# Kernel optimization log

Measured on AMD Instinct MI355X. Metric: run time of the kernel, lower is better.

Reference implementation:

```python
import jax, jax.numpy as jnp
import numpy as np

INPUT_DIM, HIDDEN_DIM, OUTPUT_DIM = 60, 256, 402


def setup_inputs() -> dict:
    key = jax.random.key(0)
    ks = jax.random.split(key, 7)
    B, T, J, D = 64, 512, 20, 3
    s_ih = 1.0 / np.sqrt(HIDDEN_DIM)
    return {
        "x": jax.random.normal(ks[0], (B, T, J, D), dtype=jnp.float32),
        "W_ih": jax.random.uniform(ks[1], (4 * HIDDEN_DIM, INPUT_DIM), minval=-s_ih, maxval=s_ih, dtype=jnp.float32),
        "W_hh": jax.random.uniform(ks[2], (4 * HIDDEN_DIM, HIDDEN_DIM), minval=-s_ih, maxval=s_ih, dtype=jnp.float32),
        "b_ih": jax.random.uniform(ks[3], (4 * HIDDEN_DIM,), minval=-s_ih, maxval=s_ih, dtype=jnp.float32),
        "b_hh": jax.random.uniform(ks[4], (4 * HIDDEN_DIM,), minval=-s_ih, maxval=s_ih, dtype=jnp.float32),
        "W_fc": jax.random.uniform(ks[5], (OUTPUT_DIM, HIDDEN_DIM), minval=-s_ih, maxval=s_ih, dtype=jnp.float32),
        "b_fc": jax.random.uniform(ks[6], (OUTPUT_DIM,), minval=-s_ih, maxval=s_ih, dtype=jnp.float32),
    }


def _lstm(x, W_ih, W_hh, b_ih, b_hh):
    # x: [B, T, INPUT_DIM] -> hidden states [B, T, H]
    B = x.shape[0]
    H = W_hh.shape[1]
    # Precompute input contribution to all gates for the whole sequence (one big GEMM)
    xg = jnp.einsum('bti,gi->btg', x, W_ih) + b_ih + b_hh  # [B, T, 4H]

    def step(carry, xt):
        h, c = carry
        gates = xt + h @ W_hh.T  # [B, 4H]; pytorch gate order: i, f, g, o
        i, f, g, o = jnp.split(gates, 4, axis=-1)
        i = jax.nn.sigmoid(i)
        f = jax.nn.sigmoid(f)
        g = jnp.tanh(g)
        o = jax.nn.sigmoid(o)
        c = f * c + i * g
        h = o * jnp.tanh(c)
        return (h, c), h

    h0 = jnp.zeros((B, H), dtype=x.dtype)
    (_, _), hs = jax.lax.scan(step, (h0, h0), jnp.swapaxes(xg, 0, 1))  # hs: [T, B, H]
    return jnp.swapaxes(hs, 0, 1)


def reference(x, W_ih, W_hh, b_ih, b_hh, W_fc, b_fc):
    B, T, J, D = x.shape
    xf = x.reshape(B, T, J * D)
    hs = _lstm(xf, W_ih, W_hh, b_ih, b_hh)  # [B, T, H]
    out = jnp.einsum('bth,oh->bto', hs, W_fc) + b_fc  # [B, T, OUTPUT_DIM]
    return out
```

## Files before the change

kernel.cpp:

```cpp
#include <hip/hip_runtime.h>
#include <hip/hip_fp16.h>

typedef _Float16 half2v __attribute__((ext_vector_type(2)));

#define B_ 64
#define T_ 512
#define H_ 256
#define G4_ 1024
#define IN_ 60
#define O_ 402

__device__ __forceinline__ float fdot2(unsigned int a, unsigned int b, float c) {
  return __builtin_amdgcn_fdot2(__builtin_bit_cast(half2v, a),
                                __builtin_bit_cast(half2v, b), c, false);
}

__device__ __forceinline__ unsigned int pack_h2(float a, float b) {
  unsigned short ua = __half_as_ushort(__float2half(a));
  unsigned short ub = __half_as_ushort(__float2half(b));
  return (unsigned int)ua | ((unsigned int)ub << 16);
}

__device__ __forceinline__ float sigmoid_f(float x) {
  return __fdividef(1.0f, 1.0f + __expf(-x));
}
__device__ __forceinline__ float tanh_f(float x) {
  float ax = fminf(fabsf(x) * 2.0f, 40.0f);
  float e = __expf(ax);
  float r = __fdividef(e - 1.0f, e + 1.0f);
  return copysignf(r, x);
}

__global__ __launch_bounds__(256) void k0_pack(
    const float* __restrict__ wih, const float* __restrict__ whh,
    const float* __restrict__ bih, const float* __restrict__ bhh,
    const float* __restrict__ wfc,
    float* __restrict__ wpih, float* __restrict__ biasp,
    unsigned int* __restrict__ wreg_ws, unsigned int* __restrict__ wlds_ws,
    unsigned int* __restrict__ wfcp) {
  int idx = blockIdx.x * 256 + threadIdx.x;
  if (idx < 61440) {
    int k = idx / 1024, rp = idx % 1024;
    int orig = (rp & 3) * 256 + (rp >> 2);
    wpih[idx] = wih[orig * IN_ + k];
  } else if (idx < 62464) {
    int rp = idx - 61440;
    int orig = (rp & 3) * 256 + (rp >> 2);
    biasp[rp] = bih[orig] + bhh[orig];
  } else if (idx < 193536) {
    int i2 = idx - 62464;
    int l = i2 >> 8;
    int i = i2 & 255;
    int cc = i >> 4, q = (i >> 2) & 3, p = i & 3;
    int u = l >> 1, hf = l & 1;
    int P = hf * 64 + cc * 4 + p;
    int row = q * 256 + u;
    unsigned int pk = pack_h2(whh[row * 256 + 2 * P], whh[row * 256 + 2 * P + 1]);
    if (cc < 12) wreg_ws[((cc * 4 + q) * 512 + l) * 4 + p] = pk;
    else         wlds_ws[(((cc - 12) * 4 + q) * 512 + l) * 4 + p] = pk;
  } else if (idx < 244992) {
    int i3 = idx - 193536;
    int o = i3 >> 7, P = i3 & 127;
    wfcp[o * 128 + P] = pack_h2(wfc[o * 256 + 2 * P], wfc[o * 256 + 2 * P + 1]);
  }
}

template <bool F32>
__global__ __launch_bounds__(256, 2) void k1_xgemm(
    const float* __restrict__ x, const float* __restrict__ wpih,
    const float* __restrict__ biasp, void* __restrict__ xg_v) {
  __shared__ float xt[IN_ * 64];
  const int l = threadIdx.x, blk = blockIdx.x;
  for (int i = l; i < IN_ * 64; i += 256) {
    int k = i >> 6, bt = i & 63;
    xt[i] = x[(size_t)(blk * 64 + bt) * IN_ + k];
  }
  __syncthreads();
  float4 bias4 = *(const float4*)&biasp[4 * l];
  float* xg_f = (float*)xg_v;
  unsigned int* xg_h = (unsigned int*)xg_v;
  for (int half = 0; half < 2; ++half) {
    float4 a[32];
#pragma unroll
    for (int j = 0; j < 32; ++j) a[j] = bias4;
    for (int k = 0; k < IN_; ++k) {
      float4 w4 = *(const float4*)&wpih[k * G4_ + 4 * l];
#pragma unroll
      for (int j4 = 0; j4 < 8; ++j4) {
        float4 xv = *(const float4*)&xt[k * 64 + half * 32 + j4 * 4];
        float xs[4] = {xv.x, xv.y, xv.z, xv.w};
#pragma unroll
        for (int jj = 0; jj < 4; ++jj) {
          float xc = xs[jj];
          float4& A = a[j4 * 4 + jj];
          A.x = fmaf(w4.x, xc, A.x); A.y = fmaf(w4.y, xc, A.y);
          A.z = fmaf(w4.z, xc, A.z); A.w = fmaf(w4.w, xc, A.w);
        }
      }
    }
#pragma unroll
    for (int j = 0; j < 32; ++j) {
      size_t bt = (size_t)blk * 64 + half * 32 + j;
      if constexpr (F32) {
        *(float4*)&xg_f[bt * G4_ + 4 * l] = a[j];
      } else {
        uint2 pk;
        pk.x = pack_h2(a[j].x, a[j].y);
        pk.y = pack_h2(a[j].z, a[j].w);
        *(uint2*)&xg_h[bt * (G4_ / 2) + 2 * l] = pk;
      }
    }
  }
}

template <bool F32>
__global__ __launch_bounds__(512, 2) void k2_lstm(
    const void* __restrict__ xg_v, const uint4* __restrict__ wreg_ws,
    const uint4* __restrict__ wlds_ws, unsigned short* __restrict__ hs) {
  __shared__ uint4 wlds[4 * 4 * 512];
  __shared__ __align__(16) unsigned short hbuf[2][256];
  const int l = threadIdx.x;
  const int b = blockIdx.x;
  const int u = l >> 1, hf = l & 1;
  for (int i = l; i < 4 * 4 * 512; i += 512) wlds[i] = wlds_ws[i];
  if (l < 128) ((unsigned int*)hbuf)[l] = 0u;

  uint4 wr[48];
#pragma unroll
  for (int i = 0; i < 48; ++i) wr[i] = wreg_ws[i * 512 + l];

  const float4* xg4 = (const float4*)xg_v;
  const uint2*  xg2 = (const uint2*)xg_v;
  float4 xf; uint2 xh;
  if constexpr (F32) xf = xg4[(size_t)b * T_ * 256 + u];
  else               xh = xg2[(size_t)b * T_ * 256 + u];
  float c = 0.0f;
  __syncthreads();
  for (int t = 0; t < T_; ++t) {
    float a0, a1, a2, a3;
    if constexpr (F32) {
      a0 = hf ? 0.0f : xf.x; a1 = hf ? 0.0f : xf.y;
      a2 = hf ? 0.0f : xf.z; a3 = hf ? 0.0f : xf.w;
    } else {
      half2v p0 = __builtin_bit_cast(half2v, xh.x);
      half2v p1 = __builtin_bit_cast(half2v, xh.y);
      a0 = hf ? 0.0f : (float)p0[0]; a1 = hf ? 0.0f : (float)p0[1];
      a2 = hf ? 0.0f : (float)p1[0]; a3 = hf ? 0.0f : (float)p1[1];
    }
    int tn = (t < T_ - 1) ? (t + 1) : t;
    if constexpr (F32) xf = xg4[(size_t)(b * T_ + tn) * 256 + u];
    else               xh = xg2[(size_t)(b * T_ + tn) * 256 + u];

    const uint4* hB = (const uint4*)(&hbuf[t & 1][hf * 128]);
#pragma unroll
    for (int cc = 0; cc < 16; ++cc) {
      uint4 hq = hB[cc];
      uint4 w0, w1, w2, w3;
      if (cc < 12) {
        w0 = wr[cc * 4 + 0]; w1 = wr[cc * 4 + 1];
        w2 = wr[cc * 4 + 2]; w3 = wr[cc * 4 + 3];
      } else {
        int c2 = cc - 12;
        w0 = wlds[(c2 * 4 + 0) * 512 + l];
        w1 = wlds[(c2 * 4 + 1) * 512 + l];
        w2 = wlds[(c2 * 4 + 2) * 512 + l];
        w3 = wlds[(c2 * 4 + 3) * 512 + l];
      }
      a0 = fdot2(w0.x, hq.x, a0); a0 = fdot2(w0.y, hq.y, a0);
      a0 = fdot2(w0.z, hq.z, a0); a0 = fdot2(w0.w, hq.w, a0);
      a1 = fdot2(w1.x, hq.x, a1); a1 = fdot2(w1.y, hq.y, a1);
      a1 = fdot2(w1.z, hq.z, a1); a1 = fdot2(w1.w, hq.w, a1);
      a2 = fdot2(w2.x, hq.x, a2); a2 = fdot2(w2.y, hq.y, a2);
      a2 = fdot2(w2.z, hq.z, a2); a2 = fdot2(w2.w, hq.w, a2);
      a3 = fdot2(w3.x, hq.x, a3); a3 = fdot2(w3.y, hq.y, a3);
      a3 = fdot2(w3.z, hq.z, a3); a3 = fdot2(w3.w, hq.w, a3);
    }
    a0 += __shfl_xor(a0, 1); a1 += __shfl_xor(a1, 1);
    a2 += __shfl_xor(a2, 1); a3 += __shfl_xor(a3, 1);
    float ig = sigmoid_f(a0), fg = sigmoid_f(a1);
    float gg = tanh_f(a2),    og = sigmoid_f(a3);
    c = fg * c + ig * gg;
    float h = og * tanh_f(c);
    unsigned short hbits = __half_as_ushort(__float2half(h));
    if (hf == 0) {
      hbuf[(t & 1) ^ 1][u] = hbits;
      hs[(size_t)(b * T_ + t) * H_ + u] = hbits;
    }
    __syncthreads();
  }
}

__global__ __launch_bounds__(256, 2) void k3_out(
    const unsigned short* __restrict__ hs, const unsigned int* __restrict__ wfcp,
    const float* __restrict__ bfc, float* __restrict__ out) {
  __shared__ unsigned int ht[64 * 128];
  const int l = threadIdx.x, blk = blockIdx.x;
  const unsigned int* hsrc = (const unsigned int*)hs + (size_t)blk * 64 * 128;
  for (int i = l; i < 64 * 128; i += 256) ht[i] = hsrc[i];
  __syncthreads();
  const int c1 = l;
  const int c2 = 256 + l;
  const bool has2 = (c2 < O_);
  const int c2r = has2 ? c2 : 0;
  float b1 = bfc[c1], b2 = bfc[c2r];
  for (int btc = 0; btc < 4; ++btc) {
    float a1[16], a2[16];
#pragma unroll
    for (int j = 0; j < 16; ++j) { a1[j] = b1; a2[j] = b2; }
    for (int Pc = 0; Pc < 8; ++Pc) {
      uint4 wq1[4], wq2[4];
#pragma unroll
      for (int p4 = 0; p4 < 4; ++p4) {
        wq1[p4] = *(const uint4*)&wfcp[c1 * 128 + Pc * 16 + 4 * p4];
        wq2[p4] = *(const uint4*)&wfcp[c2r * 128 + Pc * 16 + 4 * p4];
      }
#pragma unroll
      for (int j = 0; j < 16; ++j) {
        const unsigned int* hr = &ht[(btc * 16 + j) * 128 + Pc * 16];
#pragma unroll
        for (int p4 = 0; p4 < 4; ++p4) {
          uint4 hv = *(const uint4*)&hr[4 * p4];
          a1[j] = fdot2(wq1[p4].x, hv.x, a1[j]);
          a1[j] = fdot2(wq1[p4].y, hv.y, a1[j]);
          a1[j] = fdot2(wq1[p4].z, hv.z, a1[j]);
          a1[j] = fdot2(wq1[p4].w, hv.w, a1[j]);
          a2[j] = fdot2(wq2[p4].x, hv.x, a2[j]);
          a2[j] = fdot2(wq2[p4].y, hv.y, a2[j]);
          a2[j] = fdot2(wq2[p4].z, hv.z, a2[j]);
          a2[j] = fdot2(wq2[p4].w, hv.w, a2[j]);
        }
      }
    }
#pragma unroll
    for (int j = 0; j < 16; ++j) {
      size_t bt = (size_t)blk * 64 + btc * 16 + j;
      out[bt * O_ + c1] = a1[j];
      if (has2) out[bt * O_ + c2] = a2[j];
    }
  }
}

extern "C" void kernel_launch(void* const* d_in, const int* in_sizes, int n_in,
                              void* d_out, int out_size, void* d_ws, size_t ws_size,
                              hipStream_t stream) {
  const float* x   = (const float*)d_in[0];
  const float* wih = (const float*)d_in[1];
  const float* whh = (const float*)d_in[2];
  const float* bih = (const float*)d_in[3];
  const float* bhh = (const float*)d_in[4];
  const float* wfc = (const float*)d_in[5];
  const float* bfc = (const float*)d_in[6];
  float* out = (float*)d_out;
  char* ws = (char*)d_ws;

  const size_t HS_BYTES = (size_t)B_ * T_ * H_ * 2;
  const size_t XG_F32   = (size_t)B_ * T_ * G4_ * 4;
  const size_t WREG_B   = 12 * 4 * 512 * 16;
  const size_t WLDS_B   = 4 * 4 * 512 * 16;
  const size_t WPIH_B   = (size_t)IN_ * G4_ * 4;
  const size_t BIAS_B   = (size_t)G4_ * 4;
  const size_t WFCP_B   = (size_t)O_ * 128 * 4;
  const size_t TAIL = HS_BYTES + WREG_B + WLDS_B + WPIH_B + BIAS_B + WFCP_B;

  bool f32xg = (ws_size >= XG_F32 + TAIL);
  size_t xg_bytes = f32xg ? XG_F32 : ((size_t)B_ * T_ * G4_ * 2);

  char* xg    = ws;
  char* hsb   = ws + xg_bytes;
  char* wregp = hsb + HS_BYTES;
  char* wldsp = wregp + WREG_B;
  char* wpihp = wldsp + WLDS_B;
  char* biasp = wpihp + WPIH_B;
  char* wfcpp = biasp + BIAS_B;

  hipLaunchKernelGGL(k0_pack, dim3(957), dim3(256), 0, stream,
                     wih, whh, bih, bhh, wfc,
                     (float*)wpihp, (float*)biasp,
                     (unsigned int*)wregp, (unsigned int*)wldsp,
                     (unsigned int*)wfcpp);
  if (f32xg) {
    hipLaunchKernelGGL((k1_xgemm<true>), dim3(512), dim3(256), 0, stream,
                       x, (const float*)wpihp, (const float*)biasp, (void*)xg);
    hipLaunchKernelGGL((k2_lstm<true>), dim3(64), dim3(512), 0, stream,
                       (const void*)xg, (const uint4*)wregp, (const uint4*)wldsp,
                       (unsigned short*)hsb);
  } else {
    hipLaunchKernelGGL((k1_xgemm<false>), dim3(512), dim3(256), 0, stream,
                       x, (const float*)wpihp, (const float*)biasp, (void*)xg);
    hipLaunchKernelGGL((k2_lstm<false>), dim3(64), dim3(512), 0, stream,
                       (const void*)xg, (const uint4*)wregp, (const uint4*)wldsp,
                       (unsigned short*)hsb);
  }
  hipLaunchKernelGGL(k3_out, dim3(512), dim3(256), 0, stream,
                     (const unsigned short*)hsb, (const unsigned int*)wfcpp,
                     bfc, out);
}
```

Measured before the change: 981.5 us.

## Hold recurrent weights in AGPRs, rebalance LDS split, pack hidden-state writes

```diff
diff --git a/kernel.cpp b/kernel.cpp
--- a/kernel.cpp
+++ b/kernel.cpp
@@ -9,6 +9,9 @@
 #define G4_ 1024
 #define IN_ 60
 #define O_ 402
+
+#define NREGQ 45
+#define NLDSQ 19
 
 __device__ __forceinline__ float fdot2(unsigned int a, unsigned int b, float c) {
   return __builtin_amdgcn_fdot2(__builtin_bit_cast(half2v, a),
@@ -51,13 +54,14 @@
     int i2 = idx - 62464;
     int l = i2 >> 8;
     int i = i2 & 255;
-    int cc = i >> 4, q = (i >> 2) & 3, p = i & 3;
+    int jq = i >> 2, p = i & 3;
+    int cc = jq >> 2, q = jq & 3;
     int u = l >> 1, hf = l & 1;
     int P = hf * 64 + cc * 4 + p;
     int row = q * 256 + u;
     unsigned int pk = pack_h2(whh[row * 256 + 2 * P], whh[row * 256 + 2 * P + 1]);
-    if (cc < 12) wreg_ws[((cc * 4 + q) * 512 + l) * 4 + p] = pk;
-    else         wlds_ws[(((cc - 12) * 4 + q) * 512 + l) * 4 + p] = pk;
+    if (jq < NREGQ) wreg_ws[(jq * 512 + l) * 4 + p] = pk;
+    else            wlds_ws[((jq - NREGQ) * 512 + l) * 4 + p] = pk;
   } else if (idx < 244992) {
     int i3 = idx - 193536;
     int o = i3 >> 7, P = i3 & 127;
@@ -117,63 +121,71 @@
 __global__ __launch_bounds__(512, 2) void k2_lstm(
     const void* __restrict__ xg_v, const uint4* __restrict__ wreg_ws,
     const uint4* __restrict__ wlds_ws, unsigned short* __restrict__ hs) {
-  __shared__ uint4 wlds[4 * 4 * 512];
-  __shared__ __align__(16) unsigned short hbuf[2][256];
+  __shared__ uint4 wlds[NLDSQ * 512];
+  __shared__ unsigned int hq4[2][2][68];
   const int l = threadIdx.x;
   const int b = blockIdx.x;
   const int u = l >> 1, hf = l & 1;
-  for (int i = l; i < 4 * 4 * 512; i += 512) wlds[i] = wlds_ws[i];
-  if (l < 128) ((unsigned int*)hbuf)[l] = 0u;
-
-  uint4 wr[48];
-#pragma unroll
-  for (int i = 0; i < 48; ++i) wr[i] = wreg_ws[i * 512 + l];
-
-  const float4* xg4 = (const float4*)xg_v;
-  const uint2*  xg2 = (const uint2*)xg_v;
-  float4 xf; uint2 xh;
-  if constexpr (F32) xf = xg4[(size_t)b * T_ * 256 + u];
-  else               xh = xg2[(size_t)b * T_ * 256 + u];
+  for (int i = l; i < NLDSQ * 512; i += 512) wlds[i] = wlds_ws[i];
+  if (l < 64)        hq4[0][0][l] = 0u;
+  else if (l < 128)  hq4[0][1][l - 64] = 0u;
+
+  unsigned int wa[NREGQ * 4];
+#pragma unroll
+  for (int j = 0; j < NREGQ; ++j) {
+    uint4 v = wreg_ws[j * 512 + l];
+    asm("v_accvgpr_write_b32 %0, %1" : "=a"(wa[4 * j + 0]) : "v"(v.x));
+    asm("v_accvgpr_write_b32 %0, %1" : "=a"(wa[4 * j + 1]) : "v"(v.y));
+    asm("v_accvgpr_write_b32 %0, %1" : "=a"(wa[4 * j + 2]) : "v"(v.z));
+    asm("v_accvgpr_write_b32 %0, %1" : "=a"(wa[4 * j + 3]) : "v"(v.w));
+  }
+
+  const unsigned int* xgu = (const unsigned int*)xg_v;
+  const float2* xgf2 = (const float2*)xg_v;
+  float2 xf2; unsigned int xh;
+  if constexpr (F32) xf2 = xgf2[(size_t)b * T_ * 512 + l];
+  else               xh  = xgu[(size_t)b * T_ * 512 + l];
   float c = 0.0f;
   __syncthreads();
   for (int t = 0; t < T_; ++t) {
-    float a0, a1, a2, a3;
-    if constexpr (F32) {
-      a0 = hf ? 0.0f : xf.x; a1 = hf ? 0.0f : xf.y;
-      a2 = hf ? 0.0f : xf.z; a3 = hf ? 0.0f : xf.w;
-    } else {
-      half2v p0 = __builtin_bit_cast(half2v, xh.x);
-      half2v p1 = __builtin_bit_cast(half2v, xh.y);
-      a0 = hf ? 0.0f : (float)p0[0]; a1 = hf ? 0.0f : (float)p0[1];
-      a2 = hf ? 0.0f : (float)p1[0]; a3 = hf ? 0.0f : (float)p1[1];
-    }
+    float lo, hi;
+    if constexpr (F32) { lo = xf2.x; hi = xf2.y; }
+    else {
+      half2v p = __builtin_bit_cast(half2v, xh);
+      lo = (float)p[0]; hi = (float)p[1];
+    }
+    float a0 = hf ? 0.0f : lo, a1 = hf ? 0.0f : hi;
+    float a2 = hf ? lo : 0.0f, a3 = hf ? hi : 0.0f;
     int tn = (t < T_ - 1) ? (t + 1) : t;
-    if constexpr (F32) xf = xg4[(size_t)(b * T_ + tn) * 256 + u];
-    else               xh = xg2[(size_t)(b * T_ + tn) * 256 + u];
-
-    const uint4* hB = (const uint4*)(&hbuf[t & 1][hf * 128]);
+    if constexpr (F32) xf2 = xgf2[(size_t)(b * T_ + tn) * 512 + l];
+    else               xh  = xgu[(size_t)(b * T_ + tn) * 512 + l];
+
+    const uint4* hB = (const uint4*)hq4[t & 1][hf];
 #pragma unroll
     for (int cc = 0; cc < 16; ++cc) {
       uint4 hq = hB[cc];
-      uint4 w0, w1, w2, w3;
-      if (cc < 12) {
-        w0 = wr[cc * 4 + 0]; w1 = wr[cc * 4 + 1];
-        w2 = wr[cc * 4 + 2]; w3 = wr[cc * 4 + 3];
-      } else {
-        int c2 = cc - 12;
-        w0 = wlds[(c2 * 4 + 0) * 512 + l];
-        w1 = wlds[(c2 * 4 + 1) * 512 + l];
-        w2 = wlds[(c2 * 4 + 2) * 512 + l];
-        w3 = wlds[(c2 * 4 + 3) * 512 + l];
-      }
-      a0 = fdot2(w0.x, hq.x, a0); a0 = fdot2(w0.y, hq.y, a0);
-      a0 = fdot2(w0.z, hq.z, a0); a0 = fdot2(w0.w, hq.w, a0);
-      a1 = fdot2(w1.x, hq.x, a1); a1 = fdot2(w1.y, hq.y, a1);
-      a1 = fdot2(w1.z, hq.z, a1); a1 = fdot2(w1.w, hq.w, a1);
-      a2 = fdot2(w2.x, hq.x, a2); a2 = fdot2(w2.y, hq.y, a2);
-      a2 = fdot2(w2.z, hq.z, a2); a2 = fdot2(w2.w, hq.w, a2);
-      a3 = fdot2(w3.x, hq.x, a3); a3 = fdot2(w3.y, hq.y, a3);
-      a3 = fdot2(w3.z, hq.z, a3); a3 = fdot2(w3.w, hq.w, a3);
+      unsigned int wv[16];
+#pragma unroll
+      for (int q = 0; q < 4; ++q) {
+        int jq = cc * 4 + q;
+        if (jq < NREGQ) {
+          asm("v_accvgpr_read_b32 %0, %1" : "=v"(wv[q*4+0]) : "a"(wa[4*jq+0]), "v"(t));
+          asm("v_accvgpr_read_b32 %0, %1" : "=v"(wv[q*4+1]) : "a"(wa[4*jq+1]), "v"(t));
+          asm("v_accvgpr_read_b32 %0, %1" : "=v"(wv[q*4+2]) : "a"(wa[4*jq+2]), "v"(t));
+          asm("v_accvgpr_read_b32 %0, %1" : "=v"(wv[q*4+3]) : "a"(wa[4*jq+3]), "v"(t));
+        } else {
+          uint4 v = wlds[(jq - NREGQ) * 512 + l];
+          wv[q*4+0] = v.x; wv[q*4+1] = v.y; wv[q*4+2] = v.z; wv[q*4+3] = v.w;
+        }
+      }
+      a0 = fdot2(wv[ 0], hq.x, a0); a0 = fdot2(wv[ 1], hq.y, a0);
+      a0 = fdot2(wv[ 2], hq.z, a0); a0 = fdot2(wv[ 3], hq.w, a0);
+      a1 = fdot2(wv[ 4], hq.x, a1); a1 = fdot2(wv[ 5], hq.y, a1);
+      a1 = fdot2(wv[ 6], hq.z, a1); a1 = fdot2(wv[ 7], hq.w, a1);
+      a2 = fdot2(wv[ 8], hq.x, a2); a2 = fdot2(wv[ 9], hq.y, a2);
+      a2 = fdot2(wv[10], hq.z, a2); a2 = fdot2(wv[11], hq.w, a2);
+      a3 = fdot2(wv[12], hq.x, a3); a3 = fdot2(wv[13], hq.y, a3);
+      a3 = fdot2(wv[14], hq.z, a3); a3 = fdot2(wv[15], hq.w, a3);
     }
     a0 += __shfl_xor(a0, 1); a1 += __shfl_xor(a1, 1);
     a2 += __shfl_xor(a2, 1); a3 += __shfl_xor(a3, 1);
@@ -181,10 +193,13 @@
     float gg = tanh_f(a2),    og = sigmoid_f(a3);
     c = fg * c + ig * gg;
     float h = og * tanh_f(c);
-    unsigned short hbits = __half_as_ushort(__float2half(h));
-    if (hf == 0) {
-      hbuf[(t & 1) ^ 1][u] = hbits;
-      hs[(size_t)(b * T_ + t) * H_ + u] = hbits;
+    unsigned int hbits = (unsigned int)__half_as_ushort(__float2half(h));
+    unsigned int hnext = (unsigned int)__shfl_xor((int)hbits, 2);
+    if ((l & 3) == 0) {
+      unsigned int pk = hbits | (hnext << 16);
+      int d = l >> 2;
+      hq4[(t & 1) ^ 1][d >> 6][d & 63] = pk;
+      ((unsigned int*)hs)[(size_t)(b * T_ + t) * 128 + d] = pk;
     }
     __syncthreads();
   }
@@ -255,8 +270,8 @@
 
   const size_t HS_BYTES = (size_t)B_ * T_ * H_ * 2;
   const size_t XG_F32   = (size_t)B_ * T_ * G4_ * 4;
-  const size_t WREG_B   = 12 * 4 * 512 * 16;
-  const size_t WLDS_B   = 4 * 4 * 512 * 16;
+  const size_t WREG_B   = (size_t)NREGQ * 512 * 16;
+  const size_t WLDS_B   = (size_t)NLDSQ * 512 * 16;
   const size_t WPIH_B   = (size_t)IN_ * G4_ * 4;
   const size_t BIAS_B   = (size_t)G4_ * 4;
   const size_t WFCP_B   = (size_t)O_ * 128 * 4;
```

After: 1.387 ms. 1.41x slower.

## Split LSTM recurrence across 1024 threads with 4-way K split and streamed weights

Applied to the files above, without the earlier changes.

```diff
diff --git a/kernel.cpp b/kernel.cpp
--- a/kernel.cpp
+++ b/kernel.cpp
@@ -10,6 +10,12 @@
 #define IN_ 60
 #define O_ 402
 
+__host__ __device__ __forceinline__ constexpr int str_slot(int s, int g) {
+  int base = (s == 0) ? 0 : (2 + (s - 1) * 3);
+  int within = (s == 0) ? ((g == 0) ? 0 : 1) : g;
+  return base + within;
+}
+
 __device__ __forceinline__ float fdot2(unsigned int a, unsigned int b, float c) {
   return __builtin_amdgcn_fdot2(__builtin_bit_cast(half2v, a),
                                 __builtin_bit_cast(half2v, b), c, false);
@@ -36,7 +42,7 @@
     const float* __restrict__ bih, const float* __restrict__ bhh,
     const float* __restrict__ wfc,
     float* __restrict__ wpih, float* __restrict__ biasp,
-    unsigned int* __restrict__ wreg_ws, unsigned int* __restrict__ wlds_ws,
+    unsigned int* __restrict__ wlds_ws, unsigned int* __restrict__ wstr_ws,
     unsigned int* __restrict__ wfcp) {
   int idx = blockIdx.x * 256 + threadIdx.x;
   if (idx < 61440) {
@@ -49,15 +55,17 @@
     biasp[rp] = bih[orig] + bhh[orig];
   } else if (idx < 193536) {
     int i2 = idx - 62464;
-    int l = i2 >> 8;
-    int i = i2 & 255;
-    int cc = i >> 4, q = (i >> 2) & 3, p = i & 3;
-    int u = l >> 1, hf = l & 1;
-    int P = hf * 64 + cc * 4 + p;
-    int row = q * 256 + u;
+    int l = i2 >> 7;
+    int i = i2 & 127;
+    int jq = i >> 2, p = i & 3;
+    int s = jq >> 2, g = jq & 3;
+    int u = l >> 2, qt = l & 3;
+    int P = qt * 32 + s * 4 + p;
+    int row = g * 256 + u;
     unsigned int pk = pack_h2(whh[row * 256 + 2 * P], whh[row * 256 + 2 * P + 1]);
-    if (cc < 12) wreg_ws[((cc * 4 + q) * 512 + l) * 4 + p] = pk;
-    else         wlds_ws[(((cc - 12) * 4 + q) * 512 + l) * 4 + p] = pk;
+    if (g == 3)                wlds_ws[(s * 1024 + l) * 4 + p] = pk;
+    else if (g == 1 && s == 0) wlds_ws[(8 * 1024 + l) * 4 + p] = pk;
+    else                       wstr_ws[(str_slot(s, g) * 1024 + l) * 4 + p] = pk;
   } else if (idx < 244992) {
     int i3 = idx - 193536;
     int o = i3 >> 7, P = i3 & 127;
@@ -114,58 +122,42 @@
 }
 
 template <bool F32>
-__global__ __launch_bounds__(512, 2) void k2_lstm(
-    const void* __restrict__ xg_v, const uint4* __restrict__ wreg_ws,
-    const uint4* __restrict__ wlds_ws, unsigned short* __restrict__ hs) {
-  __shared__ uint4 wlds[4 * 4 * 512];
-  __shared__ __align__(16) unsigned short hbuf[2][256];
+__global__ __launch_bounds__(1024) void k2_lstm(
+    const void* __restrict__ xg_v, const uint4* __restrict__ wlds_ws,
+    const uint4* __restrict__ wstr_ws, unsigned short* __restrict__ hs) {
+  __shared__ uint4 wlds[9 * 1024];
+  __shared__ unsigned int hq4[2][4][36];
   const int l = threadIdx.x;
   const int b = blockIdx.x;
-  const int u = l >> 1, hf = l & 1;
-  for (int i = l; i < 4 * 4 * 512; i += 512) wlds[i] = wlds_ws[i];
-  if (l < 128) ((unsigned int*)hbuf)[l] = 0u;
-
-  uint4 wr[48];
-#pragma unroll
-  for (int i = 0; i < 48; ++i) wr[i] = wreg_ws[i * 512 + l];
-
-  const float4* xg4 = (const float4*)xg_v;
-  const uint2*  xg2 = (const uint2*)xg_v;
-  float4 xf; uint2 xh;
-  if constexpr (F32) xf = xg4[(size_t)b * T_ * 256 + u];
-  else               xh = xg2[(size_t)b * T_ * 256 + u];
+  const int qt = l & 3;
+  for (int i = l; i < 9 * 1024; i += 1024) wlds[i] = wlds_ws[i];
+  if (l < 128) hq4[0][l >> 5][l & 31] = 0u;
+
+  const unsigned short* xgu = (const unsigned short*)xg_v;
+  const float* xgf = (const float*)xg_v;
+  float xv;
+  if constexpr (F32) xv = xgf[(size_t)b * T_ * 1024 + l];
+  else               xv = (float)__builtin_bit_cast(_Float16,
+                              xgu[(size_t)b * T_ * 1024 + l]);
   float c = 0.0f;
   __syncthreads();
   for (int t = 0; t < T_; ++t) {
-    float a0, a1, a2, a3;
-    if constexpr (F32) {
-      a0 = hf ? 0.0f : xf.x; a1 = hf ? 0.0f : xf.y;
-      a2 = hf ? 0.0f : xf.z; a3 = hf ? 0.0f : xf.w;
-    } else {
-      half2v p0 = __builtin_bit_cast(half2v, xh.x);
-      half2v p1 = __builtin_bit_cast(half2v, xh.y);
-      a0 = hf ? 0.0f : (float)p0[0]; a1 = hf ? 0.0f : (float)p0[1];
-      a2 = hf ? 0.0f : (float)p1[0]; a3 = hf ? 0.0f : (float)p1[1];
-    }
+    float a0 = (qt == 0) ? xv : 0.0f, a1 = (qt == 1) ? xv : 0.0f;
+    float a2 = (qt == 2) ? xv : 0.0f, a3 = (qt == 3) ? xv : 0.0f;
     int tn = (t < T_ - 1) ? (t + 1) : t;
-    if constexpr (F32) xf = xg4[(size_t)(b * T_ + tn) * 256 + u];
-    else               xh = xg2[(size_t)(b * T_ + tn) * 256 + u];
-
-    const uint4* hB = (const uint4*)(&hbuf[t & 1][hf * 128]);
-#pragma unroll
-    for (int cc = 0; cc < 16; ++cc) {
-      uint4 hq = hB[cc];
-      uint4 w0, w1, w2, w3;
-      if (cc < 12) {
-        w0 = wr[cc * 4 + 0]; w1 = wr[cc * 4 + 1];
-        w2 = wr[cc * 4 + 2]; w3 = wr[cc * 4 + 3];
-      } else {
-        int c2 = cc - 12;
-        w0 = wlds[(c2 * 4 + 0) * 512 + l];
-        w1 = wlds[(c2 * 4 + 1) * 512 + l];
-        w2 = wlds[(c2 * 4 + 2) * 512 + l];
-        w3 = wlds[(c2 * 4 + 3) * 512 + l];
-      }
+    if constexpr (F32) xv = xgf[(size_t)(b * T_ + tn) * 1024 + l];
+    else               xv = (float)__builtin_bit_cast(_Float16,
+                                xgu[(size_t)(b * T_ + tn) * 1024 + l]);
+
+    const unsigned int* hB = hq4[t & 1][qt];
+#pragma unroll
+    for (int s = 0; s < 8; ++s) {
+      uint4 hq = *(const uint4*)&hB[s * 4];
+      uint4 w0 = wstr_ws[str_slot(s, 0) * 1024 + l];
+      uint4 w1 = (s == 0) ? wlds[8 * 1024 + l]
+                          : wstr_ws[str_slot(s, 1) * 1024 + l];
+      uint4 w2 = wstr_ws[str_slot(s, 2) * 1024 + l];
+      uint4 w3 = wlds[s * 1024 + l];
       a0 = fdot2(w0.x, hq.x, a0); a0 = fdot2(w0.y, hq.y, a0);
       a0 = fdot2(w0.z, hq.z, a0); a0 = fdot2(w0.w, hq.w, a0);
       a1 = fdot2(w1.x, hq.x, a1); a1 = fdot2(w1.y, hq.y, a1);
@@ -175,16 +167,21 @@
       a3 = fdot2(w3.x, hq.x, a3); a3 = fdot2(w3.y, hq.y, a3);
       a3 = fdot2(w3.z, hq.z, a3); a3 = fdot2(w3.w, hq.w, a3);
     }
-    a0 += __shfl_xor(a0, 1); a1 += __shfl_xor(a1, 1);
-    a2 += __shfl_xor(a2, 1); a3 += __shfl_xor(a3, 1);
+    a0 += __shfl_xor(a0, 1); a0 += __shfl_xor(a0, 2);
+    a1 += __shfl_xor(a1, 1); a1 += __shfl_xor(a1, 2);
+    a2 += __shfl_xor(a2, 1); a2 += __shfl_xor(a2, 2);
+    a3 += __shfl_xor(a3, 1); a3 += __shfl_xor(a3, 2);
     float ig = sigmoid_f(a0), fg = sigmoid_f(a1);
     float gg = tanh_f(a2),    og = sigmoid_f(a3);
     c = fg * c + ig * gg;
     float h = og * tanh_f(c);
-    unsigned short hbits = __half_as_ushort(__float2half(h));
-    if (hf == 0) {
-      hbuf[(t & 1) ^ 1][u] = hbits;
-      hs[(size_t)(b * T_ + t) * H_ + u] = hbits;
+    unsigned int hbits = (unsigned int)__half_as_ushort(__float2half(h));
+    unsigned int hnext = (unsigned int)__shfl_xor((int)hbits, 4);
+    if ((l & 7) == 0) {
+      unsigned int pk = hbits | (hnext << 16);
+      int d = l >> 3;
+      hq4[(t & 1) ^ 1][d >> 5][d & 31] = pk;
+      ((unsigned int*)hs)[(size_t)(b * T_ + t) * 128 + d] = pk;
     }
     __syncthreads();
   }
@@ -255,40 +252,40 @@
 
   const size_t HS_BYTES = (size_t)B_ * T_ * H_ * 2;
   const size_t XG_F32   = (size_t)B_ * T_ * G4_ * 4;
-  const size_t WREG_B   = 12 * 4 * 512 * 16;
-  const size_t WLDS_B   = 4 * 4 * 512 * 16;
+  const size_t WLDS_B   = (size_t)9 * 1024 * 16;
+  const size_t WSTR_B   = (size_t)23 * 1024 * 16;
   const size_t WPIH_B   = (size_t)IN_ * G4_ * 4;
   const size_t BIAS_B   = (size_t)G4_ * 4;
   const size_t WFCP_B   = (size_t)O_ * 128 * 4;
-  const size_t TAIL = HS_BYTES + WREG_B + WLDS_B + WPIH_B + BIAS_B + WFCP_B;
+  const size_t TAIL = HS_BYTES + WLDS_B + WSTR_B + WPIH_B + BIAS_B + WFCP_B;
 
   bool f32xg = (ws_size >= XG_F32 + TAIL);
   size_t xg_bytes = f32xg ? XG_F32 : ((size_t)B_ * T_ * G4_ * 2);
 
   char* xg    = ws;
   char* hsb   = ws + xg_bytes;
-  char* wregp = hsb + HS_BYTES;
-  char* wldsp = wregp + WREG_B;
-  char* wpihp = wldsp + WLDS_B;
+  char* wldsp = hsb + HS_BYTES;
+  char* wstrp = wldsp + WLDS_B;
+  char* wpihp = wstrp + WSTR_B;
   char* biasp = wpihp + WPIH_B;
   char* wfcpp = biasp + BIAS_B;
 
   hipLaunchKernelGGL(k0_pack, dim3(957), dim3(256), 0, stream,
                      wih, whh, bih, bhh, wfc,
                      (float*)wpihp, (float*)biasp,
-                     (unsigned int*)wregp, (unsigned int*)wldsp,
+                     (unsigned int*)wldsp, (unsigned int*)wstrp,
                      (unsigned int*)wfcpp);
   if (f32xg) {
     hipLaunchKernelGGL((k1_xgemm<true>), dim3(512), dim3(256), 0, stream,
                        x, (const float*)wpihp, (const float*)biasp, (void*)xg);
-    hipLaunchKernelGGL((k2_lstm<true>), dim3(64), dim3(512), 0, stream,
-                       (const void*)xg, (const uint4*)wregp, (const uint4*)wldsp,
+    hipLaunchKernelGGL((k2_lstm<true>), dim3(64), dim3(1024), 0, stream,
+                       (const void*)xg, (const uint4*)wldsp, (const uint4*)wstrp,
                        (unsigned short*)hsb);
   } else {
     hipLaunchKernelGGL((k1_xgemm<false>), dim3(512), dim3(256), 0, stream,
                        x, (const float*)wpihp, (const float*)biasp, (void*)xg);
-    hipLaunchKernelGGL((k2_lstm<false>), dim3(64), dim3(512), 0, stream,
-                       (const void*)xg, (const uint4*)wregp, (const uint4*)wldsp,
+    hipLaunchKernelGGL((k2_lstm<false>), dim3(64), dim3(1024), 0, stream,
+                       (const void*)xg, (const uint4*)wldsp, (const uint4*)wstrp,
                        (unsigned short*)hsb);
   }
   hipLaunchKernelGGL(k3_out, dim3(512), dim3(256), 0, stream,
```

After: 1.183 ms. 20.5% more time.
